# Optimization experiments

Hardware: AMD Instinct MI355X
Metric: run time of the kernel (lower is better)

The kernel has to match this reference:

```python
import jax, jax.numpy as jnp
import numpy as np

HEADS = 8
DIM_HEAD = 64
LN_EPS = 1e-5


def _layernorm(x, gamma, beta):
    mu = jnp.mean(x, axis=-1, keepdims=True)
    var = jnp.var(x, axis=-1, keepdims=True)
    return (x - mu) * jax.lax.rsqrt(var + LN_EPS) * gamma + beta


def setup_inputs() -> dict:
    key = jax.random.key(0)
    ks = jax.random.split(key, 5)
    B, N, D = 1, 16384, 512
    return {
        "x": jax.random.normal(ks[0], (B, N, D), dtype=jnp.float32),
        "ln_gamma": jnp.ones((D,), dtype=jnp.float32),
        "ln_beta": jnp.zeros((D,), dtype=jnp.float32),
        "w_qkv": jax.random.normal(ks[1], (D, 3 * D), dtype=jnp.float32) * (D ** -0.5),
        "agent": jax.random.normal(ks[2], (HEADS, 512, DIM_HEAD), dtype=jnp.float32) * (DIM_HEAD ** -0.5),
        "w_out": jax.random.normal(ks[3], (D, D), dtype=jnp.float32) * (D ** -0.5),
        "b_out": jnp.zeros((D,), dtype=jnp.float32),
    }


def reference(x, ln_gamma, ln_beta, w_qkv, agent, w_out, b_out):
    # TransLayer: x + Mask_Agent_Attention(LayerNorm(x))
    B, N, D = x.shape
    xn = _layernorm(x, ln_gamma, ln_beta)

    qkv = xn @ w_qkv                                   # [B, N, 3D]
    q, k, v = jnp.split(qkv, 3, axis=-1)
    # [B, H, N, d]
    q = q.reshape(B, N, HEADS, DIM_HEAD).transpose(0, 2, 1, 3)
    k = k.reshape(B, N, HEADS, DIM_HEAD).transpose(0, 2, 1, 3)
    v = v.reshape(B, N, HEADS, DIM_HEAD).transpose(0, 2, 1, 3)

    scale = DIM_HEAD ** -0.5  # tem=0 -> classical 1/sqrt(d) scaling

    # agents aggregate values: softmax over keys  [B, H, A, N]
    attn1 = jax.nn.softmax(jnp.einsum('had,bhnd->bhan', agent, k) * scale, axis=-1)
    agent_v = jnp.einsum('bhan,bhnd->bhad', attn1, v)  # [B, H, A, d]

    # queries attend to agents: softmax over agents  [B, H, N, A]
    attn2 = jax.nn.softmax(jnp.einsum('bhnd,had->bhna', q, agent) * scale, axis=-1)
    out = jnp.einsum('bhna,bhad->bhnd', attn2, agent_v)  # [B, H, N, d]

    out = out + v  # residual=True: value residual inside attention
    out = out.transpose(0, 2, 1, 3).reshape(B, N, D)
    out = out @ w_out + b_out
    return x + out
```

## Files before the change

kernel.cpp:

```cpp
#include <hip/hip_runtime.h>
#include <stdint.h>

typedef unsigned short u16;
typedef __attribute__((ext_vector_type(8))) short bf16x8;
typedef __attribute__((ext_vector_type(4))) float f32x4;

__device__ __forceinline__ float bf2f(u16 u){
  union { uint32_t i; float f; } v; v.i = ((uint32_t)u) << 16; return v.f;
}
__device__ __forceinline__ u16 f2bf(float f){
  union { float fl; uint32_t i; } v; v.fl = f;
  uint32_t r = v.i + 0x7FFFu + ((v.i >> 16) & 1u);
  return (u16)(r >> 16);
}
__device__ __forceinline__ uint32_t cvt_pk_bf16(float lo, float hi){
  uint32_t r;
  asm("v_cvt_pk_bf16_f32 %0, %1, %2" : "=v"(r) : "v"(lo), "v"(hi));
  return r;
}
__device__ __forceinline__ f32x4 mfma16(bf16x8 a, bf16x8 b, f32x4 c){
  return __builtin_amdgcn_mfma_f32_16x16x32_bf16(a, b, c, 0, 0, 0);
}
__device__ __forceinline__ void gload16(const u16* g, u16* l){
  __builtin_amdgcn_global_load_lds((const __attribute__((address_space(1))) void*)g,
                                   (__attribute__((address_space(3))) void*)l, 16, 0, 0);
}

__global__ __launch_bounds__(256) void k_conv_bf(const float* __restrict__ in, u16* __restrict__ out, int n, float scale){
  int i = (blockIdx.x * 256 + threadIdx.x) * 4;
  if (i >= n) return;
  float4 v = *(const float4*)(in + i);
  ushort4 o; o.x=f2bf(v.x*scale); o.y=f2bf(v.y*scale); o.z=f2bf(v.z*scale); o.w=f2bf(v.w*scale);
  *(ushort4*)(out + i) = o;
}

__global__ __launch_bounds__(256) void k_transp(const float* __restrict__ in, u16* __restrict__ out, int R, int C){
  __shared__ u16 tile[64][68];
  int c0 = blockIdx.x * 64, r0 = blockIdx.y * 64;
  int tr = threadIdx.x >> 4;
  int tc = (threadIdx.x & 15) * 4;
  for (int rr = 0; rr < 4; rr++){
    int r = rr * 16 + tr;
    float4 v = *(const float4*)(in + (size_t)(r0 + r) * C + c0 + tc);
    ushort4 o; o.x=f2bf(v.x); o.y=f2bf(v.y); o.z=f2bf(v.z); o.w=f2bf(v.w);
    *(ushort4*)&tile[r][tc] = o;
  }
  __syncthreads();
  for (int rr = 0; rr < 4; rr++){
    int oc = rr * 16 + tr;
    ushort4 o;
    o.x = tile[tc+0][oc]; o.y = tile[tc+1][oc]; o.z = tile[tc+2][oc]; o.w = tile[tc+3][oc];
    *(ushort4*)(out + (size_t)(c0 + oc) * R + r0 + tc) = o;
  }
}

__global__ __launch_bounds__(256) void k_transp_v(const u16* __restrict__ qkv, u16* __restrict__ vT){
  __shared__ u16 tile[64][68];
  int n0 = blockIdx.x * 64;
  int c0 = blockIdx.y * 64;
  int tr = threadIdx.x >> 4;
  int tc = (threadIdx.x & 15) * 4;
  for (int rr = 0; rr < 4; rr++){
    int r = rr * 16 + tr;
    ushort4 v = *(const ushort4*)(qkv + (size_t)(n0 + r) * 1536 + 1024 + c0 + tc);
    *(ushort4*)&tile[r][tc] = v;
  }
  __syncthreads();
  for (int rr = 0; rr < 4; rr++){
    int oc = rr * 16 + tr;
    ushort4 o;
    o.x = tile[tc+0][oc]; o.y = tile[tc+1][oc]; o.z = tile[tc+2][oc]; o.w = tile[tc+3][oc];
    *(ushort4*)(vT + (size_t)(c0 + oc) * 16384 + n0 + tc) = o;
  }
}

__global__ __launch_bounds__(128) void k_ln(const float* __restrict__ x, const float* __restrict__ g,
                                            const float* __restrict__ b, u16* __restrict__ xn){
  int row = blockIdx.x;
  int t = threadIdx.x;
  float4 v = *(const float4*)(x + (size_t)row * 512 + t * 4);
  float s = v.x + v.y + v.z + v.w;
  float q = v.x*v.x + v.y*v.y + v.z*v.z + v.w*v.w;
  for (int o = 32; o > 0; o >>= 1){ s += __shfl_down(s, o); q += __shfl_down(q, o); }
  __shared__ float red[4];
  if ((t & 63) == 0){ red[(t >> 6) * 2] = s; red[(t >> 6) * 2 + 1] = q; }
  __syncthreads();
  float mu  = (red[0] + red[2]) * (1.0f/512.0f);
  float var = (red[1] + red[3]) * (1.0f/512.0f) - mu * mu;
  float rs = rsqrtf(var + 1e-5f);
  float4 gv = *(const float4*)(g + t * 4);
  float4 bv = *(const float4*)(b + t * 4);
  ushort4 o;
  o.x = f2bf((v.x - mu) * rs * gv.x + bv.x);
  o.y = f2bf((v.y - mu) * rs * gv.y + bv.y);
  o.z = f2bf((v.z - mu) * rs * gv.z + bv.z);
  o.w = f2bf((v.w - mu) * rs * gv.w + bv.w);
  *(ushort4*)(xn + (size_t)row * 512 + t * 4) = o;
}

__global__ __launch_bounds__(256) void k_gemm_qkv(const u16* __restrict__ A, const u16* __restrict__ Bt,
                                                  u16* __restrict__ C){
  __shared__ u16 aL[2][128 * 64];
  __shared__ u16 bL[2][128 * 64];
  int m0 = blockIdx.x * 128, n0 = blockIdx.y * 128;
  int t = threadIdx.x, w = t >> 6, l = t & 63;
  int wm = (w >> 1) * 64, wn = (w & 1) * 64;
  int lr = l & 15, kb0 = (l >> 4) * 8;
  const u16* gA = A  + (size_t)(m0 + w*32 + (l >> 3)) * 512 + (l & 7) * 8;
  const u16* gB = Bt + (size_t)(n0 + w*32 + (l >> 3)) * 512 + (l & 7) * 8;
  int ldsOff = (w*32) * 64;
  f32x4 acc[4][4];
  for (int i=0;i<4;i++) for (int j=0;j<4;j++) acc[i][j] = {0.f,0.f,0.f,0.f};

  auto stage = [&](int buf, int k0){
    #pragma unroll
    for (int i = 0; i < 4; i++){
      gload16(gA + k0 + (size_t)i*8*512, &aL[buf][ldsOff + i*8*64]);
      gload16(gB + k0 + (size_t)i*8*512, &bL[buf][ldsOff + i*8*64]);
    }
  };
  auto comp = [&](const u16* ab, const u16* bb){
    #pragma unroll
    for (int kk = 0; kk < 64; kk += 32){
      int kb = kb0 + kk;
      bf16x8 av[4], bv[4];
      #pragma unroll
      for (int mt=0;mt<4;mt++) av[mt] = *(const bf16x8*)&ab[(wm + mt*16 + lr)*64 + kb];
      #pragma unroll
      for (int nt=0;nt<4;nt++) bv[nt] = *(const bf16x8*)&bb[(wn + nt*16 + lr)*64 + kb];
      #pragma unroll
      for (int mt=0;mt<4;mt++)
        #pragma unroll
        for (int nt=0;nt<4;nt++)
          acc[mt][nt] = mfma16(av[mt], bv[nt], acc[mt][nt]);
    }
  };

  stage(0, 0);
  __syncthreads();
  #pragma unroll
  for (int tk = 0; tk < 8; tk += 2){
    stage(1, (tk + 1) * 64);
    comp(&aL[0][0], &bL[0][0]);
    __syncthreads();
    if (tk + 2 < 8) stage(0, (tk + 2) * 64);
    comp(&aL[1][0], &bL[1][0]);
    __syncthreads();
  }

  int rr = (l >> 4) * 4, cc = l & 15;
  for (int mt=0;mt<4;mt++) for (int nt=0;nt<4;nt++)
    for (int j=0;j<4;j++){
      int r = m0 + wm + mt*16 + rr + j;
      int c = n0 + wn + nt*16 + cc;
      C[(size_t)r * 1536 + c] = f2bf(acc[mt][nt][j]);
    }
}

__global__ __launch_bounds__(256) void k_gemm_out(const u16* __restrict__ A, const u16* __restrict__ Bt,
                                                  const float* __restrict__ x, const float* __restrict__ bias,
                                                  float* __restrict__ y){
  __shared__ u16 aL[2][128 * 64];
  __shared__ u16 bL[2][128 * 64];
  int m0 = blockIdx.x * 128, n0 = blockIdx.y * 128;
  int t = threadIdx.x, w = t >> 6, l = t & 63;
  int wm = (w >> 1) * 64, wn = (w & 1) * 64;
  int lr = l & 15, kb0 = (l >> 4) * 8;
  const u16* gA = A  + (size_t)(m0 + w*32 + (l >> 3)) * 512 + (l & 7) * 8;
  const u16* gB = Bt + (size_t)(n0 + w*32 + (l >> 3)) * 512 + (l & 7) * 8;
  int ldsOff = (w*32) * 64;
  f32x4 acc[4][4];
  for (int i=0;i<4;i++) for (int j=0;j<4;j++) acc[i][j] = {0.f,0.f,0.f,0.f};

  auto stage = [&](int buf, int k0){
    #pragma unroll
    for (int i = 0; i < 4; i++){
      gload16(gA + k0 + (size_t)i*8*512, &aL[buf][ldsOff + i*8*64]);
      gload16(gB + k0 + (size_t)i*8*512, &bL[buf][ldsOff + i*8*64]);
    }
  };
  auto comp = [&](const u16* ab, const u16* bb){
    #pragma unroll
    for (int kk = 0; kk < 64; kk += 32){
      int kb = kb0 + kk;
      bf16x8 av[4], bv[4];
      #pragma unroll
      for (int mt=0;mt<4;mt++) av[mt] = *(const bf16x8*)&ab[(wm + mt*16 + lr)*64 + kb];
      #pragma unroll
      for (int nt=0;nt<4;nt++) bv[nt] = *(const bf16x8*)&bb[(wn + nt*16 + lr)*64 + kb];
      #pragma unroll
      for (int mt=0;mt<4;mt++)
        #pragma unroll
        for (int nt=0;nt<4;nt++)
          acc[mt][nt] = mfma16(av[mt], bv[nt], acc[mt][nt]);
    }
  };

  stage(0, 0);
  __syncthreads();
  #pragma unroll
  for (int tk = 0; tk < 8; tk += 2){
    stage(1, (tk + 1) * 64);
    comp(&aL[0][0], &bL[0][0]);
    __syncthreads();
    if (tk + 2 < 8) stage(0, (tk + 2) * 64);
    comp(&aL[1][0], &bL[1][0]);
    __syncthreads();
  }

  int rr = (l >> 4) * 4, cc = l & 15;
  for (int mt=0;mt<4;mt++) for (int nt=0;nt<4;nt++)
    for (int j=0;j<4;j++){
      int r = m0 + wm + mt*16 + rr + j;
      int c = n0 + wn + nt*16 + cc;
      y[(size_t)r * 512 + c] = acc[mt][nt][j] + bias[c] + x[(size_t)r * 512 + c];
    }
}

__global__ __launch_bounds__(256) void k_agent_agg(const u16* __restrict__ agbf, const u16* __restrict__ qkv,
                                                   const u16* __restrict__ vT,
                                                   float* __restrict__ nump, float* __restrict__ denp){
  int L = blockIdx.x;
  int g = (L >> 6) * 8 + (L & 7);
  int m = (L >> 3) & 7;
  int h = g >> 4, ch = g & 15, a0 = m * 64;

  __shared__ u16 ag[64][72];
  __shared__ u16 kt[64][72];
  __shared__ u16 vt[64][72];
  __shared__ u16 pt[64][72];
  int t = threadIdx.x, w = t >> 6, l = t & 63;

  for (int i = 0; i < 2; i++){
    int flat = t + 256 * i;
    int r = flat >> 3, c = (flat & 7) * 8;
    *(uint4*)&ag[r][c] = *(const uint4*)(agbf + (size_t)(h * 512 + a0 + r) * 64 + c);
  }

  bf16x8 ones;
  for (int i = 0; i < 8; i++) ones[i] = (short)0x3F80;

  f32x4 acc2[4];
  for (int i=0;i<4;i++) acc2[i] = {0.f,0.f,0.f,0.f};
  f32x4 accd = {0.f,0.f,0.f,0.f};

  for (int sub = 0; sub < 16; sub++){
    int n0 = ch * 1024 + sub * 64;
    __syncthreads();
    {
      int flat = t;
      int r = flat >> 3, c = (flat & 7) * 8;
      *(uint4*)&kt[r][c] = *(const uint4*)(qkv + (size_t)(n0 + r) * 1536 + 512 + h * 64 + c);
      int flat2 = t + 256;
      int r2 = flat2 >> 3, c2 = (flat2 & 7) * 8;
      *(uint4*)&kt[r2][c2] = *(const uint4*)(qkv + (size_t)(n0 + r2) * 1536 + 512 + h * 64 + c2);
      *(uint4*)&vt[r][c]   = *(const uint4*)(vT + ((size_t)(h * 64 + r) << 14) + n0 + c);
      *(uint4*)&vt[r2][c2] = *(const uint4*)(vT + ((size_t)(h * 64 + r2) << 14) + n0 + c2);
    }
    __syncthreads();

    f32x4 s[4];
    for (int nt=0;nt<4;nt++) s[nt] = {0.f,0.f,0.f,0.f};
    for (int kk = 0; kk < 64; kk += 32){
      int kb = kk + (l >> 4) * 8;
      bf16x8 kf = *(const bf16x8*)&kt[w*16 + (l & 15)][kb];
      for (int nt=0;nt<4;nt++){
        bf16x8 af = *(const bf16x8*)&ag[nt*16 + (l & 15)][kb];
        s[nt] = mfma16(kf, af, s[nt]);
      }
    }
    int nb = w*16 + (l >> 4) * 4;
    for (int nt=0;nt<4;nt++){
      int a = nt*16 + (l & 15);
      uint32_t w0 = cvt_pk_bf16(__builtin_amdgcn_exp2f(s[nt][0]), __builtin_amdgcn_exp2f(s[nt][1]));
      uint32_t w1 = cvt_pk_bf16(__builtin_amdgcn_exp2f(s[nt][2]), __builtin_amdgcn_exp2f(s[nt][3]));
      uint2 o; o.x = w0; o.y = w1;
      *(uint2*)&pt[a][nb] = o;
    }
    __syncthreads();

    for (int kk = 0; kk < 64; kk += 32){
      int kb = kk + (l >> 4) * 8;
      bf16x8 vf = *(const bf16x8*)&vt[w*16 + (l & 15)][kb];
      for (int mt=0;mt<4;mt++){
        bf16x8 pf = *(const bf16x8*)&pt[mt*16 + (l & 15)][kb];
        acc2[mt] = mfma16(pf, vf, acc2[mt]);
      }
      bf16x8 pw = *(const bf16x8*)&pt[w*16 + (l & 15)][kb];
      accd = mfma16(ones, pw, accd);
    }
  }

  size_t base = ((size_t)(h * 16 + ch) * 512 + a0) * 64;
  for (int mt=0;mt<4;mt++)
    #pragma unroll
    for (int j=0;j<4;j++){
      int a = mt*16 + (l>>4)*4 + j;
      int d = w*16 + (l&15);
      nump[base + (size_t)a*64 + d] = acc2[mt][j];
    }
  if (l < 16) denp[(size_t)(h*16 + ch) * 512 + a0 + w*16 + l] = accd[0];
}

__global__ __launch_bounds__(64) void k_agent_reduce(const float* __restrict__ nump, const float* __restrict__ denp,
                                                     u16* __restrict__ avtg){
  int h = blockIdx.x >> 9;
  int a = blockIdx.x & 511;
  int d = threadIdx.x;
  float num = 0.f, den = 0.f;
  for (int c = 0; c < 16; c++){
    num += nump[((size_t)(h * 16 + c) * 512 + a) * 64 + d];
    den += denp[(size_t)(h * 16 + c) * 512 + a];
  }
  avtg[((size_t)h * 64 + d) * 512 + a] = f2bf(num / den);
}

__global__ __launch_bounds__(256) void k_qattn(const u16* __restrict__ qkv, const u16* __restrict__ agbf,
                                               const u16* __restrict__ avtg, u16* __restrict__ atto){
  int n0 = blockIdx.x * 64;
  int h  = blockIdx.y;
  __shared__ u16 qt[64][72];
  __shared__ u16 ag[64][72];
  __shared__ u16 avt[64][72];
  __shared__ u16 pt[64][72];
  __shared__ float dnf[64];
  int t = threadIdx.x, w = t >> 6, l = t & 63;

  for (int i = 0; i < 2; i++){
    int flat = t + 256 * i;
    int r = flat >> 3, c = (flat & 7) * 8;
    *(uint4*)&qt[r][c] = *(const uint4*)(qkv + (size_t)(n0 + r) * 1536 + h * 64 + c);
  }

  bf16x8 ones;
  for (int i = 0; i < 8; i++) ones[i] = (short)0x3F80;

  f32x4 acc[4];
  for (int i=0;i<4;i++) acc[i] = {0.f,0.f,0.f,0.f};
  f32x4 accd = {0.f,0.f,0.f,0.f};

  for (int at = 0; at < 8; at++){
    int a0 = at * 64;
    __syncthreads();
    for (int i = 0; i < 2; i++){
      int flat = t + 256 * i;
      int r = flat >> 3, c = (flat & 7) * 8;
      *(uint4*)&ag[r][c]  = *(const uint4*)(agbf + (size_t)(h * 512 + a0 + r) * 64 + c);
      *(uint4*)&avt[r][c] = *(const uint4*)(avtg + (size_t)(h * 64 + r) * 512 + a0 + c);
    }
    __syncthreads();

    f32x4 s[4];
    for (int nt=0;nt<4;nt++) s[nt] = {0.f,0.f,0.f,0.f};
    for (int kk = 0; kk < 64; kk += 32){
      int kb = kk + (l >> 4) * 8;
      bf16x8 af = *(const bf16x8*)&ag[w*16 + (l & 15)][kb];
      for (int nt=0;nt<4;nt++){
        bf16x8 qf = *(const bf16x8*)&qt[nt*16 + (l & 15)][kb];
        s[nt] = mfma16(af, qf, s[nt]);
      }
    }
    int ab = w*16 + (l >> 4) * 4;
    for (int nt=0;nt<4;nt++){
      int n = nt*16 + (l & 15);
      uint32_t w0 = cvt_pk_bf16(__builtin_amdgcn_exp2f(s[nt][0]), __builtin_amdgcn_exp2f(s[nt][1]));
      uint32_t w1 = cvt_pk_bf16(__builtin_amdgcn_exp2f(s[nt][2]), __builtin_amdgcn_exp2f(s[nt][3]));
      uint2 o; o.x = w0; o.y = w1;
      *(uint2*)&pt[n][ab] = o;
    }
    __syncthreads();

    for (int kk = 0; kk < 64; kk += 32){
      int kb = kk + (l >> 4) * 8;
      bf16x8 vf = *(const bf16x8*)&avt[w*16 + (l & 15)][kb];
      for (int mt=0;mt<4;mt++){
        bf16x8 pf = *(const bf16x8*)&pt[mt*16 + (l & 15)][kb];
        acc[mt] = mfma16(pf, vf, acc[mt]);
      }
      bf16x8 pw = *(const bf16x8*)&pt[w*16 + (l & 15)][kb];
      accd = mfma16(ones, pw, accd);
    }
  }

  if (l < 16) dnf[w*16 + l] = accd[0];
  __syncthreads();
  if (t < 64) dnf[t] = __builtin_amdgcn_rcpf(dnf[t]);
  __syncthreads();

  int d = w*16 + (l & 15);
  for (int mt=0;mt<4;mt++){
    #pragma unroll
    for (int j=0;j<4;j++){
      int n = mt*16 + (l>>4)*4 + j;
      float v = bf2f(qkv[(size_t)(n0 + n) * 1536 + 1024 + h * 64 + d]);
      atto[(size_t)(n0 + n) * 512 + h * 64 + d] = f2bf(acc[mt][j] * dnf[n] + v);
    }
  }
}

extern "C" void kernel_launch(void* const* d_in, const int* in_sizes, int n_in,
                              void* d_out, int out_size, void* d_ws, size_t ws_size,
                              hipStream_t stream) {
  const float* x     = (const float*)d_in[0];
  const float* gamma = (const float*)d_in[1];
  const float* beta  = (const float*)d_in[2];
  const float* w_qkv = (const float*)d_in[3];
  const float* agent = (const float*)d_in[4];
  const float* w_out = (const float*)d_in[5];
  const float* b_out = (const float*)d_in[6];
  float* y = (float*)d_out;

  char* ws = (char*)d_ws;
  u16*   xn    = (u16*)  (ws + 0);
  u16*   vT    = (u16*)  (ws + 0);
  u16*   qkv   = (u16*)  (ws + 16777216);
  u16*   wqkvt = (u16*)  (ws + 67108864);
  u16*   woutt = (u16*)  (ws + 68681728);
  u16*   agbf  = (u16*)  (ws + 69206016);
  u16*   avtg  = (u16*)  (ws + 69730304);
  u16*   atto  = (u16*)  (ws + 70254592);
  float* nump  = (float*)(ws + 87031808);
  float* denp  = (float*)(ws + 103809024);

  k_conv_bf   <<<dim3(256),     dim3(256), 0, stream>>>(agent, agbf, 8*512*64, 0.125f * 1.44269504089f);
  k_transp    <<<dim3(24, 8),   dim3(256), 0, stream>>>(w_qkv, wqkvt, 512, 1536);
  k_transp    <<<dim3(8, 8),    dim3(256), 0, stream>>>(w_out, woutt, 512, 512);
  k_ln        <<<dim3(16384),   dim3(128), 0, stream>>>(x, gamma, beta, xn);
  k_gemm_qkv  <<<dim3(128, 12), dim3(256), 0, stream>>>(xn, wqkvt, qkv);
  k_transp_v  <<<dim3(256, 8),  dim3(256), 0, stream>>>(qkv, vT);
  k_agent_agg <<<dim3(1024),    dim3(256), 0, stream>>>(agbf, qkv, vT, nump, denp);
  k_agent_reduce<<<dim3(4096),  dim3(64),  0, stream>>>(nump, denp, avtg);
  k_qattn     <<<dim3(256, 8),  dim3(256), 0, stream>>>(qkv, agbf, avtg, atto);
  k_gemm_out  <<<dim3(128, 4),  dim3(256), 0, stream>>>(atto, woutt, x, b_out, y);
}
```

Measured before the change: 182.1 us.

## Use 256x128 GEMM tiles with 8 waves and XOR-swizzled LDS layout

```diff
diff --git a/kernel.cpp b/kernel.cpp
--- a/kernel.cpp
+++ b/kernel.cpp
@@ -98,36 +98,38 @@
   *(ushort4*)(xn + (size_t)row * 512 + t * 4) = o;
 }
 
-__global__ __launch_bounds__(256) void k_gemm_qkv(const u16* __restrict__ A, const u16* __restrict__ Bt,
+
+__global__ __launch_bounds__(512) void k_gemm_qkv(const u16* __restrict__ A, const u16* __restrict__ Bt,
                                                   u16* __restrict__ C){
-  __shared__ u16 aL[2][128 * 64];
+  __shared__ u16 aL[2][256 * 64];
   __shared__ u16 bL[2][128 * 64];
-  int m0 = blockIdx.x * 128, n0 = blockIdx.y * 128;
+  int m0 = blockIdx.x * 256, n0 = blockIdx.y * 128;
   int t = threadIdx.x, w = t >> 6, l = t & 63;
   int wm = (w >> 1) * 64, wn = (w & 1) * 64;
-  int lr = l & 15, kb0 = (l >> 4) * 8;
-  const u16* gA = A  + (size_t)(m0 + w*32 + (l >> 3)) * 512 + (l & 7) * 8;
-  const u16* gB = Bt + (size_t)(n0 + w*32 + (l >> 3)) * 512 + (l & 7) * 8;
-  int ldsOff = (w*32) * 64;
+  int lr = l & 15;
+  int blkSrc = (l & 7) ^ ((l >> 3) & 7);
+  const u16* gA = A  + (size_t)(m0 + w*8 + (l >> 3)) * 512 + blkSrc * 8;
+  const u16* gB = Bt + (size_t)(n0 + w*8 + (l >> 3)) * 512 + blkSrc * 8;
   f32x4 acc[4][4];
   for (int i=0;i<4;i++) for (int j=0;j<4;j++) acc[i][j] = {0.f,0.f,0.f,0.f};
 
   auto stage = [&](int buf, int k0){
     #pragma unroll
-    for (int i = 0; i < 4; i++){
-      gload16(gA + k0 + (size_t)i*8*512, &aL[buf][ldsOff + i*8*64]);
-      gload16(gB + k0 + (size_t)i*8*512, &bL[buf][ldsOff + i*8*64]);
-    }
+    for (int p = 0; p < 4; p++)
+      gload16(gA + (size_t)p*64*512 + k0, &aL[buf][(p*64 + w*8) * 64]);
+    #pragma unroll
+    for (int p = 0; p < 2; p++)
+      gload16(gB + (size_t)p*64*512 + k0, &bL[buf][(p*64 + w*8) * 64]);
   };
   auto comp = [&](const u16* ab, const u16* bb){
     #pragma unroll
     for (int kk = 0; kk < 64; kk += 32){
-      int kb = kb0 + kk;
+      int xo = (((l >> 4) + (kk >> 3)) ^ (l & 7)) << 3;
       bf16x8 av[4], bv[4];
       #pragma unroll
-      for (int mt=0;mt<4;mt++) av[mt] = *(const bf16x8*)&ab[(wm + mt*16 + lr)*64 + kb];
-      #pragma unroll
-      for (int nt=0;nt<4;nt++) bv[nt] = *(const bf16x8*)&bb[(wn + nt*16 + lr)*64 + kb];
+      for (int mt=0;mt<4;mt++) av[mt] = *(const bf16x8*)&ab[(wm + mt*16 + lr)*64 + xo];
+      #pragma unroll
+      for (int nt=0;nt<4;nt++) bv[nt] = *(const bf16x8*)&bb[(wn + nt*16 + lr)*64 + xo];
       #pragma unroll
       for (int mt=0;mt<4;mt++)
         #pragma unroll
@@ -139,12 +141,10 @@
   stage(0, 0);
   __syncthreads();
   #pragma unroll
-  for (int tk = 0; tk < 8; tk += 2){
-    stage(1, (tk + 1) * 64);
-    comp(&aL[0][0], &bL[0][0]);
-    __syncthreads();
-    if (tk + 2 < 8) stage(0, (tk + 2) * 64);
-    comp(&aL[1][0], &bL[1][0]);
+  for (int tk = 0; tk < 8; tk++){
+    int cur = tk & 1;
+    if (tk < 7) stage(cur ^ 1, (tk + 1) * 64);
+    comp(&aL[cur][0], &bL[cur][0]);
     __syncthreads();
   }
 
@@ -157,37 +157,38 @@
     }
 }
 
-__global__ __launch_bounds__(256) void k_gemm_out(const u16* __restrict__ A, const u16* __restrict__ Bt,
+__global__ __launch_bounds__(512) void k_gemm_out(const u16* __restrict__ A, const u16* __restrict__ Bt,
                                                   const float* __restrict__ x, const float* __restrict__ bias,
                                                   float* __restrict__ y){
-  __shared__ u16 aL[2][128 * 64];
+  __shared__ u16 aL[2][256 * 64];
   __shared__ u16 bL[2][128 * 64];
-  int m0 = blockIdx.x * 128, n0 = blockIdx.y * 128;
+  int m0 = blockIdx.x * 256, n0 = blockIdx.y * 128;
   int t = threadIdx.x, w = t >> 6, l = t & 63;
   int wm = (w >> 1) * 64, wn = (w & 1) * 64;
-  int lr = l & 15, kb0 = (l >> 4) * 8;
-  const u16* gA = A  + (size_t)(m0 + w*32 + (l >> 3)) * 512 + (l & 7) * 8;
-  const u16* gB = Bt + (size_t)(n0 + w*32 + (l >> 3)) * 512 + (l & 7) * 8;
-  int ldsOff = (w*32) * 64;
+  int lr = l & 15;
+  int blkSrc = (l & 7) ^ ((l >> 3) & 7);
+  const u16* gA = A  + (size_t)(m0 + w*8 + (l >> 3)) * 512 + blkSrc * 8;
+  const u16* gB = Bt + (size_t)(n0 + w*8 + (l >> 3)) * 512 + blkSrc * 8;
   f32x4 acc[4][4];
   for (int i=0;i<4;i++) for (int j=0;j<4;j++) acc[i][j] = {0.f,0.f,0.f,0.f};
 
   auto stage = [&](int buf, int k0){
     #pragma unroll
-    for (int i = 0; i < 4; i++){
-      gload16(gA + k0 + (size_t)i*8*512, &aL[buf][ldsOff + i*8*64]);
-      gload16(gB + k0 + (size_t)i*8*512, &bL[buf][ldsOff + i*8*64]);
-    }
+    for (int p = 0; p < 4; p++)
+      gload16(gA + (size_t)p*64*512 + k0, &aL[buf][(p*64 + w*8) * 64]);
+    #pragma unroll
+    for (int p = 0; p < 2; p++)
+      gload16(gB + (size_t)p*64*512 + k0, &bL[buf][(p*64 + w*8) * 64]);
   };
   auto comp = [&](const u16* ab, const u16* bb){
     #pragma unroll
     for (int kk = 0; kk < 64; kk += 32){
-      int kb = kb0 + kk;
+      int xo = (((l >> 4) + (kk >> 3)) ^ (l & 7)) << 3;
       bf16x8 av[4], bv[4];
       #pragma unroll
-      for (int mt=0;mt<4;mt++) av[mt] = *(const bf16x8*)&ab[(wm + mt*16 + lr)*64 + kb];
-      #pragma unroll
-      for (int nt=0;nt<4;nt++) bv[nt] = *(const bf16x8*)&bb[(wn + nt*16 + lr)*64 + kb];
+      for (int mt=0;mt<4;mt++) av[mt] = *(const bf16x8*)&ab[(wm + mt*16 + lr)*64 + xo];
+      #pragma unroll
+      for (int nt=0;nt<4;nt++) bv[nt] = *(const bf16x8*)&bb[(wn + nt*16 + lr)*64 + xo];
       #pragma unroll
       for (int mt=0;mt<4;mt++)
         #pragma unroll
@@ -199,12 +200,10 @@
   stage(0, 0);
   __syncthreads();
   #pragma unroll
-  for (int tk = 0; tk < 8; tk += 2){
-    stage(1, (tk + 1) * 64);
-    comp(&aL[0][0], &bL[0][0]);
-    __syncthreads();
-    if (tk + 2 < 8) stage(0, (tk + 2) * 64);
-    comp(&aL[1][0], &bL[1][0]);
+  for (int tk = 0; tk < 8; tk++){
+    int cur = tk & 1;
+    if (tk < 7) stage(cur ^ 1, (tk + 1) * 64);
+    comp(&aL[cur][0], &bL[cur][0]);
     __syncthreads();
   }
 
@@ -426,10 +425,10 @@
   k_transp    <<<dim3(24, 8),   dim3(256), 0, stream>>>(w_qkv, wqkvt, 512, 1536);
   k_transp    <<<dim3(8, 8),    dim3(256), 0, stream>>>(w_out, woutt, 512, 512);
   k_ln        <<<dim3(16384),   dim3(128), 0, stream>>>(x, gamma, beta, xn);
-  k_gemm_qkv  <<<dim3(128, 12), dim3(256), 0, stream>>>(xn, wqkvt, qkv);
+  k_gemm_qkv  <<<dim3(64, 12),  dim3(512), 0, stream>>>(xn, wqkvt, qkv);
   k_transp_v  <<<dim3(256, 8),  dim3(256), 0, stream>>>(qkv, vT);
   k_agent_agg <<<dim3(1024),    dim3(256), 0, stream>>>(agbf, qkv, vT, nump, denp);
   k_agent_reduce<<<dim3(4096),  dim3(64),  0, stream>>>(nump, denp, avtg);
   k_qattn     <<<dim3(256, 8),  dim3(256), 0, stream>>>(qkv, agbf, avtg, atto);
-  k_gemm_out  <<<dim3(128, 4),  dim3(256), 0, stream>>>(atto, woutt, x, b_out, y);
-}
+  k_gemm_out  <<<dim3(64, 4),   dim3(512), 0, stream>>>(atto, woutt, x, b_out, y);
+}
```

Measured after the change: 167.6 us. 1.09x faster.
